# Kernel tuning notes

Measured on AMD Instinct MI355X. Metric: run time of the kernel, lower is better.

The kernel has to match this reference:

```python
import jax, jax.numpy as jnp
import numpy as np

R, C, N, E, H, F, ED, G, L = 1, 4, 50000, 200000, 128, 128, 16, 64, 2


def setup_inputs() -> dict:
    key = jax.random.key(0)
    ks = jax.random.split(key, 16)
    s = 0.05
    return {
        "x": jax.random.normal(ks[0], (R * C * N, H), jnp.float32),
        "batch": jnp.sort(jax.random.randint(ks[1], (N,), 0, G)),
        "edge_index": jax.random.randint(ks[2], (2, E), 0, N),
        "edge_attr": jax.random.normal(ks[3], (1, 1, E, ED), jnp.float32),
        "node_mask": jax.random.uniform(ks[4], (R, C, N, 1), jnp.float32),
        "edge_mask": jax.random.uniform(ks[5], (R, C, E, 1), jnp.float32),
        "W_be": jax.random.normal(ks[6], (ED, H), jnp.float32) * s,
        "b_be": jnp.zeros((H,), jnp.float32),
        "eps": jnp.zeros((L,), jnp.float32),
        "W1": jax.random.normal(ks[7], (L, H, H), jnp.float32) * s,
        "b1": jnp.zeros((L, H), jnp.float32),
        "W2": jax.random.normal(ks[8], (L, H, H), jnp.float32) * s,
        "b2": jnp.zeros((L, H), jnp.float32),
        "Wm1": jax.random.normal(ks[9], (H, H), jnp.float32) * s,
        "bm1": jnp.zeros((H,), jnp.float32),
        "Wm2": jax.random.normal(ks[10], (H, F), jnp.float32) * s,
        "bm2": jnp.zeros((F,), jnp.float32),
    }


def reference(x, batch, edge_index, edge_attr, node_mask, edge_mask,
              W_be, b_be, eps, W1, b1, W2, b2, Wm1, bm1, Wm2, bm2):
    gelu = lambda v: jax.nn.gelu(v, approximate=False)  # torch F.gelu default is erf
    src, dst = edge_index[0], edge_index[1]
    # bond encoder, shared across conv layers: (1,1,E,H)
    ee = edge_attr @ W_be + b_be
    for l in range(L):
        ux = x.reshape(R, C, N, H)
        # gather + add + GELU + edge-weight multiply: (R,C,E,H)
        msg = gelu(ux[:, :, src, :] + ee) * edge_mask
        # scatter_sum over edges into destination nodes
        agg = jnp.zeros_like(ux).at[:, :, dst, :].add(msg)
        h = (1.0 + eps[l]) * x + agg.reshape(x.shape)
        # conv MLP: Linear -> GELU -> Linear, then outer GELU (norm=Identity, dropout=0)
        h = gelu(h @ W1[l] + b1[l]) @ W2[l] + b2[l]
        x = gelu(h)
    # final node MLP (PyG MLP, norm=None): Linear -> GELU -> Linear
    x = gelu(x @ Wm1 + bm1) @ Wm2 + bm2  # (R*C*N, F)
    x4 = x.reshape(R, C, N, F)
    # masked mean-pool per (repeat, centroid, graph)
    num = jnp.zeros((R, C, G, F), x.dtype).at[:, :, batch, :].add(x4 * node_mask)
    den = jnp.zeros((R, C, G, 1), x.dtype).at[:, :, batch, :].add(node_mask) + 1e-7
    pooled = (num / den).transpose(0, 2, 1, 3).reshape(-1, F)  # (R*G*C, F)
    return pooled
```

## Files before the change

kernel.cpp:

```cpp
#include <hip/hip_runtime.h>
#include <math.h>

#define NN 50000
#define EN 200000
#define CC 4
#define HH 128
#define GG 64
#define LDSA 136
#define LDSF 132

typedef __attribute__((ext_vector_type(8))) short bs8;
typedef __attribute__((ext_vector_type(4))) float f32x4;
typedef __attribute__((ext_vector_type(2))) float f32x2;

__device__ __forceinline__ unsigned short f2bf(float f) {
  unsigned int u = __float_as_uint(f);
  u += 0x7FFFu + ((u >> 16) & 1u);
  return (unsigned short)(u >> 16);
}
__device__ __forceinline__ float bf2f(unsigned short h) {
  return __uint_as_float(((unsigned int)h) << 16);
}
__device__ __forceinline__ float gelu_f(float x) {
  float z = fabsf(x) * 0.7071067811865476f;
  float t = __builtin_amdgcn_rcpf(fmaf(0.3275911f, z, 1.0f));
  float poly = t * fmaf(t, fmaf(t, fmaf(t, fmaf(t, 1.061405429f, -1.453152027f),
                                        1.421413741f), -0.284496736f), 0.254829592f);
  float e = fmaf(-poly, __expf(-z * z), 1.0f);
  return 0.5f * x * (1.0f + copysignf(e, x));
}
__device__ __forceinline__ float gelu2_f(float x) {
  float z = fabsf(x) * 0.7071067811865476f;
  float t = __builtin_amdgcn_rcpf(fmaf(0.3275911f, z, 1.0f));
  float poly = t * fmaf(t, fmaf(t, fmaf(t, fmaf(t, 1.061405429f, -1.453152027f),
                                        1.421413741f), -0.284496736f), 0.254829592f);
  float e = fmaf(-poly, __expf(-z * z), 1.0f);
  return x * (1.0f + copysignf(e, x));
}

__global__ __launch_bounds__(256) void count_kernel(const int* __restrict__ dst,
                                                    int* __restrict__ counts) {
  int e = blockIdx.x * 256 + threadIdx.x;
  if (e < EN) atomicAdd(&counts[dst[e]], 1);
}

__global__ __launch_bounds__(256) void block_sum_kernel(const int* __restrict__ counts,
                                                        int* __restrict__ bsums) {
  int tid = threadIdx.x;
  int i = blockIdx.x * 256 + tid;
  int v = (i < NN) ? counts[i] : 0;
#pragma unroll
  for (int d = 1; d < 64; d <<= 1) v += __shfl_xor(v, d);
  __shared__ int ws4[4];
  if ((tid & 63) == 0) ws4[tid >> 6] = v;
  __syncthreads();
  if (tid == 0) bsums[blockIdx.x] = ws4[0] + ws4[1] + ws4[2] + ws4[3];
}

__global__ __launch_bounds__(256) void bsum_scan_kernel(const int* __restrict__ bsums,
                                                        int* __restrict__ boffs, int nb) {
  int tid = threadIdx.x, lane = tid & 63, wv = tid >> 6;
  int v = (tid < nb) ? bsums[tid] : 0;
  int s = v;
#pragma unroll
  for (int d = 1; d < 64; d <<= 1) { int t = __shfl_up(s, d); if (lane >= d) s += t; }
  __shared__ int wsum[4];
  if (lane == 63) wsum[wv] = s;
  __syncthreads();
  int pre = 0;
  for (int j = 0; j < wv; ++j) pre += wsum[j];
  if (tid < nb) boffs[tid] = pre + s - v;
}

__global__ __launch_bounds__(256) void block_scan_kernel(const int* __restrict__ counts,
                                                         const int* __restrict__ boffs,
                                                         int* __restrict__ offsets,
                                                         int* __restrict__ cursor) {
  int tid = threadIdx.x, lane = tid & 63, wv = tid >> 6;
  int i = blockIdx.x * 256 + tid;
  int v = (i < NN) ? counts[i] : 0;
  int s = v;
#pragma unroll
  for (int d = 1; d < 64; d <<= 1) { int t = __shfl_up(s, d); if (lane >= d) s += t; }
  __shared__ int wsum[4];
  if (lane == 63) wsum[wv] = s;
  __syncthreads();
  int pre = boffs[blockIdx.x];
  for (int j = 0; j < wv; ++j) pre += wsum[j];
  if (i < NN) { int e = pre + s - v; offsets[i] = e; cursor[i] = e; }
  if (i == 0) offsets[NN] = EN;
}

__global__ __launch_bounds__(256) void fill_kernel(const int* __restrict__ dst,
                                                   const int* __restrict__ src,
                                                   const float* __restrict__ emask,
                                                   int* __restrict__ cursor,
                                                   int2* __restrict__ csr_es,
                                                   float4* __restrict__ emask_s) {
  int e = blockIdx.x * 256 + threadIdx.x;
  if (e < EN) {
    int s = src[e];
    float m0 = emask[e];
    float m1 = emask[EN + e];
    float m2 = emask[2 * EN + e];
    float m3 = emask[3 * EN + e];
    int pos = atomicAdd(&cursor[dst[e]], 1);
    csr_es[pos] = make_int2(e, s);
    emask_s[pos] = make_float4(m0, m1, m2, m3);
  }
}

__global__ __launch_bounds__(256) void prep_w_kernel(const float* __restrict__ W1,
                                                     const float* __restrict__ W2,
                                                     const float* __restrict__ Wm1,
                                                     const float* __restrict__ Wm2,
                                                     unsigned short* __restrict__ wts) {
  int m = blockIdx.x >> 6;
  int idx = (blockIdx.x & 63) * 256 + threadIdx.x;
  const float* src = (m == 0) ? W1 : (m == 1) ? W1 + 16384 : (m == 2) ? W2
                     : (m == 3) ? W2 + 16384 : (m == 4) ? Wm1 : Wm2;
  unsigned short* dhi = wts + m * 32768;
  unsigned short* dlo = dhi + 16384;
  int n = idx >> 7, k = idx & 127;
  float v = src[k * HH + n];
  unsigned short hi = f2bf(v);
  dhi[n * HH + k] = hi;
  dlo[n * HH + k] = f2bf(v - bf2f(hi));
}

__global__ __launch_bounds__(256) void ee_kernel(const float* __restrict__ eattr,
                                                 const float* __restrict__ Wbe,
                                                 const float* __restrict__ bbe,
                                                 float* __restrict__ ee) {
  __shared__ float Ws[16 * HH];
  __shared__ float Ea[16 * 16];
  int tid = threadIdx.x;
  int e0 = blockIdx.x * 16;
#pragma unroll
  for (int i = 0; i < 8; ++i) Ws[tid + i * 256] = Wbe[tid + i * 256];
  Ea[tid] = eattr[(size_t)e0 * 16 + tid];
  __syncthreads();
  int h = tid & 127, half = tid >> 7;
  float bb = bbe[h];
#pragma unroll
  for (int j = 0; j < 8; ++j) {
    int el = j * 2 + half;
    float acc = bb;
#pragma unroll
    for (int d = 0; d < 16; ++d) acc += Ea[el * 16 + d] * Ws[d * HH + h];
    ee[(size_t)(e0 + el) * HH + h] = acc;
  }
}

__global__ __launch_bounds__(256) void agg_kernel(const float* __restrict__ x,
                                                  const float* __restrict__ ee,
                                                  const int* __restrict__ off,
                                                  const int2* __restrict__ csr_es,
                                                  const float4* __restrict__ emask_s,
                                                  const float* __restrict__ epsp, int layer,
                                                  float* __restrict__ hout) {
  int wv = threadIdx.x >> 6, lane = threadIdx.x & 63;
  int v = blockIdx.x * 4 + wv;
  int c2 = lane * 2;
  float2 acc[CC];
#pragma unroll
  for (int c = 0; c < CC; ++c) { acc[c].x = 0.f; acc[c].y = 0.f; }
  int beg = off[v], end = off[v + 1];

  float2 eeC; float2 xC[CC]; float emC[CC];
  int2 esN = make_int2(0, 0);
  eeC.x = 0.f; eeC.y = 0.f;
#pragma unroll
  for (int c = 0; c < CC; ++c) { xC[c].x = 0.f; xC[c].y = 0.f; emC[c] = 0.f; }

  if (beg < end) {
    int2 es0 = csr_es[beg];
    eeC = *(const float2*)(ee + (size_t)es0.x * HH + c2);
#pragma unroll
    for (int c = 0; c < CC; ++c)
      xC[c] = *(const float2*)(x + ((size_t)c * NN + es0.y) * HH + c2);
    float4 m = emask_s[beg];
    emC[0] = 0.5f * m.x; emC[1] = 0.5f * m.y; emC[2] = 0.5f * m.z; emC[3] = 0.5f * m.w;
    if (beg + 1 < end) esN = csr_es[beg + 1];
  }

  for (int t = beg; t < end; ++t) {
    float2 eeB; float2 xB[CC]; float emB[CC];
    int2 esNN = make_int2(0, 0);
    if (t + 1 < end) {
      eeB = *(const float2*)(ee + (size_t)esN.x * HH + c2);
#pragma unroll
      for (int c = 0; c < CC; ++c)
        xB[c] = *(const float2*)(x + ((size_t)c * NN + esN.y) * HH + c2);
      float4 m = emask_s[t + 1];
      emB[0] = 0.5f * m.x; emB[1] = 0.5f * m.y; emB[2] = 0.5f * m.z; emB[3] = 0.5f * m.w;
      if (t + 2 < end) esNN = csr_es[t + 2];
    } else {
      eeB.x = 0.f; eeB.y = 0.f;
#pragma unroll
      for (int c = 0; c < CC; ++c) { xB[c].x = 0.f; xB[c].y = 0.f; emB[c] = 0.f; }
    }
#pragma unroll
    for (int c = 0; c < CC; ++c) {
      acc[c].x += gelu2_f(xC[c].x + eeC.x) * emC[c];
      acc[c].y += gelu2_f(xC[c].y + eeC.y) * emC[c];
    }
    eeC = eeB;
#pragma unroll
    for (int c = 0; c < CC; ++c) { xC[c] = xB[c]; emC[c] = emB[c]; }
    esN = esNN;
  }

  float ep = 1.0f + epsp[layer];
#pragma unroll
  for (int c = 0; c < CC; ++c) {
    float2 xs = *(const float2*)(x + ((size_t)c * NN + v) * HH + c2);
    f32x2 o;
    o[0] = fmaf(ep, xs.x, acc[c].x);
    o[1] = fmaf(ep, xs.y, acc[c].y);
    __builtin_nontemporal_store(o, (f32x2*)(hout + ((size_t)c * NN + v) * HH + c2));
  }
}

__global__ __launch_bounds__(256, 2) void mlp_kernel(
    const float* __restrict__ in,
    const unsigned short* __restrict__ w1hi, const unsigned short* __restrict__ w1lo,
    const float* __restrict__ b1,
    const unsigned short* __restrict__ w2hi, const unsigned short* __restrict__ w2lo,
    const float* __restrict__ b2,
    float* __restrict__ out) {
  __shared__ __align__(16) unsigned short AB[2 * 64 * HH];
  unsigned short* Ahi = AB;
  unsigned short* Alo = AB + 64 * HH;
  int tid = threadIdx.x;
  int row0 = blockIdx.x * 64;
  int lane = tid & 63, wq = tid >> 6;
  int ln = lane & 15, quad = lane >> 4;

  bs8 b1h[4][2], b1l[4][2];
#pragma unroll
  for (int ks = 0; ks < 4; ++ks)
#pragma unroll
    for (int nt = 0; nt < 2; ++nt) {
      int wrow = ((wq * 2 + nt) * 16 + ln) * HH + ks * 32 + quad * 8;
      b1h[ks][nt] = *(const bs8*)(w1hi + wrow);
      b1l[ks][nt] = *(const bs8*)(w1lo + wrow);
    }

#pragma unroll
  for (int i = 0; i < 4; ++i) {
    int idx = tid + i * 256;
    int r = idx >> 4, blk = idx & 15;
    const float* p = in + (size_t)(row0 + r) * HH + blk * 8;
    f32x4 v0 = __builtin_nontemporal_load((const f32x4*)p);
    f32x4 v1 = __builtin_nontemporal_load((const f32x4*)(p + 4));
    bs8 h, l;
    h[0] = f2bf(v0[0]); h[1] = f2bf(v0[1]); h[2] = f2bf(v0[2]); h[3] = f2bf(v0[3]);
    h[4] = f2bf(v1[0]); h[5] = f2bf(v1[1]); h[6] = f2bf(v1[2]); h[7] = f2bf(v1[3]);
    l[0] = f2bf(v0[0] - bf2f(h[0])); l[1] = f2bf(v0[1] - bf2f(h[1]));
    l[2] = f2bf(v0[2] - bf2f(h[2])); l[3] = f2bf(v0[3] - bf2f(h[3]));
    l[4] = f2bf(v1[0] - bf2f(h[4])); l[5] = f2bf(v1[1] - bf2f(h[5]));
    l[6] = f2bf(v1[2] - bf2f(h[6])); l[7] = f2bf(v1[3] - bf2f(h[7]));
    int sb = blk ^ (r & 15);
    *(bs8*)(Ahi + r * HH + sb * 8) = h;
    *(bs8*)(Alo + r * HH + sb * 8) = l;
  }
  __syncthreads();

  f32x4 acc[4][2];
#pragma unroll
  for (int mt = 0; mt < 4; ++mt)
#pragma unroll
    for (int nt = 0; nt < 2; ++nt)
#pragma unroll
      for (int r = 0; r < 4; ++r) acc[mt][nt][r] = 0.f;
#pragma unroll
  for (int ks = 0; ks < 4; ++ks) {
    bs8 ah[4], al[4];
    int sb = ((ks * 4 + quad) ^ ln) * 8;
#pragma unroll
    for (int mt = 0; mt < 4; ++mt) {
      ah[mt] = *(const bs8*)(Ahi + (mt * 16 + ln) * HH + sb);
      al[mt] = *(const bs8*)(Alo + (mt * 16 + ln) * HH + sb);
    }
#pragma unroll
    for (int nt = 0; nt < 2; ++nt)
#pragma unroll
      for (int mt = 0; mt < 4; ++mt) {
        acc[mt][nt] = __builtin_amdgcn_mfma_f32_16x16x32_bf16(al[mt], b1h[ks][nt], acc[mt][nt], 0, 0, 0);
        acc[mt][nt] = __builtin_amdgcn_mfma_f32_16x16x32_bf16(ah[mt], b1l[ks][nt], acc[mt][nt], 0, 0, 0);
        acc[mt][nt] = __builtin_amdgcn_mfma_f32_16x16x32_bf16(ah[mt], b1h[ks][nt], acc[mt][nt], 0, 0, 0);
      }
  }
  __syncthreads();

  bs8 b2h[4][2], b2l[4][2];
#pragma unroll
  for (int ks = 0; ks < 4; ++ks)
#pragma unroll
    for (int nt = 0; nt < 2; ++nt) {
      int wrow = ((wq * 2 + nt) * 16 + ln) * HH + ks * 32 + quad * 8;
      b2h[ks][nt] = *(const bs8*)(w2hi + wrow);
      b2l[ks][nt] = *(const bs8*)(w2lo + wrow);
    }

#pragma unroll
  for (int nt = 0; nt < 2; ++nt) {
    int col = (wq * 2 + nt) * 16 + ln;
    int cb = col >> 3, co = col & 7;
    float bb = b1[col];
#pragma unroll
    for (int mt = 0; mt < 4; ++mt)
#pragma unroll
      for (int r = 0; r < 4; ++r) {
        float tv = gelu_f(acc[mt][nt][r] + bb);
        unsigned short th = f2bf(tv);
        int rr = mt * 16 + quad * 4 + r;
        int sof = rr * HH + (cb ^ (rr & 15)) * 8 + co;
        Ahi[sof] = th;
        Alo[sof] = f2bf(tv - bf2f(th));
      }
  }
  __syncthreads();

#pragma unroll
  for (int mt = 0; mt < 4; ++mt)
#pragma unroll
    for (int nt = 0; nt < 2; ++nt)
#pragma unroll
      for (int r = 0; r < 4; ++r) acc[mt][nt][r] = 0.f;
#pragma unroll
  for (int ks = 0; ks < 4; ++ks) {
    bs8 ah[4], al[4];
    int sb = ((ks * 4 + quad) ^ ln) * 8;
#pragma unroll
    for (int mt = 0; mt < 4; ++mt) {
      ah[mt] = *(const bs8*)(Ahi + (mt * 16 + ln) * HH + sb);
      al[mt] = *(const bs8*)(Alo + (mt * 16 + ln) * HH + sb);
    }
#pragma unroll
    for (int nt = 0; nt < 2; ++nt)
#pragma unroll
      for (int mt = 0; mt < 4; ++mt) {
        acc[mt][nt] = __builtin_amdgcn_mfma_f32_16x16x32_bf16(al[mt], b2h[ks][nt], acc[mt][nt], 0, 0, 0);
        acc[mt][nt] = __builtin_amdgcn_mfma_f32_16x16x32_bf16(ah[mt], b2l[ks][nt], acc[mt][nt], 0, 0, 0);
        acc[mt][nt] = __builtin_amdgcn_mfma_f32_16x16x32_bf16(ah[mt], b2h[ks][nt], acc[mt][nt], 0, 0, 0);
      }
  }
#pragma unroll
  for (int nt = 0; nt < 2; ++nt) {
    int col = (wq * 2 + nt) * 16 + ln;
    float bb = b2[col];
#pragma unroll
    for (int mt = 0; mt < 4; ++mt)
#pragma unroll
      for (int r = 0; r < 4; ++r) {
        float o = gelu_f(acc[mt][nt][r] + bb);
        out[(size_t)(row0 + mt * 16 + quad * 4 + r) * HH + col] = o;
      }
  }
}

__global__ __launch_bounds__(256, 2) void mlp_pool_kernel(
    const float* __restrict__ in,
    const unsigned short* __restrict__ w1hi, const unsigned short* __restrict__ w1lo,
    const float* __restrict__ b1,
    const unsigned short* __restrict__ w2hi, const unsigned short* __restrict__ w2lo,
    const float* __restrict__ b2,
    const float* __restrict__ nmask, const int* __restrict__ batch,
    float* __restrict__ num) {
  __shared__ __align__(16) unsigned short AB[128 * LDSA];
  __shared__ int kk[64];
  unsigned short* Ahi = AB;
  unsigned short* Alo = AB + 64 * LDSA;
  int tid = threadIdx.x;
  int row0 = blockIdx.x * 64;
  int lane = tid & 63, wq = tid >> 6;
  int ln = lane & 15, quad = lane >> 4;

  bs8 b1h[4][2], b1l[4][2];
#pragma unroll
  for (int ks = 0; ks < 4; ++ks)
#pragma unroll
    for (int nt = 0; nt < 2; ++nt) {
      int wrow = ((wq * 2 + nt) * 16 + ln) * HH + ks * 32 + quad * 8;
      b1h[ks][nt] = *(const bs8*)(w1hi + wrow);
      b1l[ks][nt] = *(const bs8*)(w1lo + wrow);
    }
#pragma unroll
  for (int i = 0; i < 8; ++i) {
    int idx = tid + i * 256;
    int r = idx >> 5, cc4 = idx & 31;
    f32x4 vv = __builtin_nontemporal_load(
        (const f32x4*)(in + (size_t)(row0 + r) * HH + cc4 * 4));
    unsigned short h0 = f2bf(vv[0]), h1 = f2bf(vv[1]), h2 = f2bf(vv[2]), h3 = f2bf(vv[3]);
    ushort4 hv; hv.x = h0; hv.y = h1; hv.z = h2; hv.w = h3;
    ushort4 lv;
    lv.x = f2bf(vv[0] - bf2f(h0)); lv.y = f2bf(vv[1] - bf2f(h1));
    lv.z = f2bf(vv[2] - bf2f(h2)); lv.w = f2bf(vv[3] - bf2f(h3));
    *(ushort4*)(Ahi + r * LDSA + cc4 * 4) = hv;
    *(ushort4*)(Alo + r * LDSA + cc4 * 4) = lv;
  }
  if (tid < 64) {
    int gr = row0 + tid;
    int c = gr / NN;
    int n = gr - c * NN;
    kk[tid] = (c << 6) | batch[n];
  }
  __syncthreads();

  f32x4 acc[4][2];
#pragma unroll
  for (int mt = 0; mt < 4; ++mt)
#pragma unroll
    for (int nt = 0; nt < 2; ++nt)
#pragma unroll
      for (int r = 0; r < 4; ++r) acc[mt][nt][r] = 0.f;
#pragma unroll
  for (int ks = 0; ks < 4; ++ks) {
    bs8 ah[4], al[4];
#pragma unroll
    for (int mt = 0; mt < 4; ++mt) {
      ah[mt] = *(const bs8*)(Ahi + (mt * 16 + ln) * LDSA + ks * 32 + quad * 8);
      al[mt] = *(const bs8*)(Alo + (mt * 16 + ln) * LDSA + ks * 32 + quad * 8);
    }
#pragma unroll
    for (int nt = 0; nt < 2; ++nt)
#pragma unroll
      for (int mt = 0; mt < 4; ++mt) {
        acc[mt][nt] = __builtin_amdgcn_mfma_f32_16x16x32_bf16(al[mt], b1h[ks][nt], acc[mt][nt], 0, 0, 0);
        acc[mt][nt] = __builtin_amdgcn_mfma_f32_16x16x32_bf16(ah[mt], b1l[ks][nt], acc[mt][nt], 0, 0, 0);
        acc[mt][nt] = __builtin_amdgcn_mfma_f32_16x16x32_bf16(ah[mt], b1h[ks][nt], acc[mt][nt], 0, 0, 0);
      }
  }
  __syncthreads();

  bs8 b2h[4][2], b2l[4][2];
#pragma unroll
  for (int ks = 0; ks < 4; ++ks)
#pragma unroll
    for (int nt = 0; nt < 2; ++nt) {
      int wrow = ((wq * 2 + nt) * 16 + ln) * HH + ks * 32 + quad * 8;
      b2h[ks][nt] = *(const bs8*)(w2hi + wrow);
      b2l[ks][nt] = *(const bs8*)(w2lo + wrow);
    }
#pragma unroll
  for (int nt = 0; nt < 2; ++nt) {
    int col = (wq * 2 + nt) * 16 + ln;
    float bb = b1[col];
#pragma unroll
    for (int mt = 0; mt < 4; ++mt)
#pragma unroll
      for (int r = 0; r < 4; ++r) {
        float tv = gelu_f(acc[mt][nt][r] + bb);
        unsigned short th = f2bf(tv);
        int rr = mt * 16 + quad * 4 + r;
        Ahi[rr * LDSA + col] = th;
        Alo[rr * LDSA + col] = f2bf(tv - bf2f(th));
      }
  }
  __syncthreads();

#pragma unroll
  for (int mt = 0; mt < 4; ++mt)
#pragma unroll
    for (int nt = 0; nt < 2; ++nt)
#pragma unroll
      for (int r = 0; r < 4; ++r) acc[mt][nt][r] = 0.f;
#pragma unroll
  for (int ks = 0; ks < 4; ++ks) {
    bs8 ah[4], al[4];
#pragma unroll
    for (int mt = 0; mt < 4; ++mt) {
      ah[mt] = *(const bs8*)(Ahi + (mt * 16 + ln) * LDSA + ks * 32 + quad * 8);
      al[mt] = *(const bs8*)(Alo + (mt * 16 + ln) * LDSA + ks * 32 + quad * 8);
    }
#pragma unroll
    for (int nt = 0; nt < 2; ++nt)
#pragma unroll
      for (int mt = 0; mt < 4; ++mt) {
        acc[mt][nt] = __builtin_amdgcn_mfma_f32_16x16x32_bf16(al[mt], b2h[ks][nt], acc[mt][nt], 0, 0, 0);
        acc[mt][nt] = __builtin_amdgcn_mfma_f32_16x16x32_bf16(ah[mt], b2l[ks][nt], acc[mt][nt], 0, 0, 0);
        acc[mt][nt] = __builtin_amdgcn_mfma_f32_16x16x32_bf16(ah[mt], b2h[ks][nt], acc[mt][nt], 0, 0, 0);
      }
  }
  __syncthreads();
  float* Tf = (float*)AB;
#pragma unroll
  for (int nt = 0; nt < 2; ++nt) {
    int col = (wq * 2 + nt) * 16 + ln;
    float bb = b2[col];
#pragma unroll
    for (int mt = 0; mt < 4; ++mt)
#pragma unroll
      for (int r = 0; r < 4; ++r) {
        int rl = mt * 16 + quad * 4 + r;
        int gr = row0 + rl;
        Tf[rl * LDSF + col] = (acc[mt][nt][r] + bb) * nmask[gr];
      }
  }
  __syncthreads();
  if (tid < 128) {
    int col = tid;
    float a2 = 0.f;
    int cur = kk[0];
    for (int r = 0; r < 64; ++r) {
      int k2 = kk[r];
      if (k2 != cur) {
        atomicAdd(&num[((size_t)(cur & 63) * CC + (cur >> 6)) * HH + col], a2);
        a2 = 0.f;
        cur = k2;
      }
      a2 += Tf[r * LDSF + col];
    }
    atomicAdd(&num[((size_t)(cur & 63) * CC + (cur >> 6)) * HH + col], a2);
  }
}

__global__ __launch_bounds__(256) void pool_finalize_kernel(const float* __restrict__ num,
                                                            const int* __restrict__ batch,
                                                            const float* __restrict__ nmask,
                                                            float* __restrict__ outp) {
  int g = blockIdx.x >> 2, c = blockIdx.x & 3;
  int lo = 0, hi = NN;
  while (lo < hi) { int m = (lo + hi) >> 1; if (batch[m] < g) lo = m + 1; else hi = m; }
  int start = lo;
  hi = NN;
  while (lo < hi) { int m = (lo + hi) >> 1; if (batch[m] < g + 1) lo = m + 1; else hi = m; }
  int end = lo;
  int tid = threadIdx.x;
  float d = 0.f;
  for (int n = start + tid; n < end; n += 256) d += nmask[c * NN + n];
#pragma unroll
  for (int k = 1; k < 64; k <<= 1) d += __shfl_xor(d, k);
  __shared__ float ws4[4];
  if ((tid & 63) == 0) ws4[tid >> 6] = d;
  __syncthreads();
  float den = ws4[0] + ws4[1] + ws4[2] + ws4[3] + 1e-7f;
  if (tid < 128) {
    int idx = blockIdx.x * 128 + tid;
    outp[idx] = num[idx] / den;
  }
}

extern "C" void kernel_launch(void* const* d_in, const int* in_sizes, int n_in,
                              void* d_out, int out_size, void* d_ws, size_t ws_size,
                              hipStream_t stream) {
  const float* x_in  = (const float*)d_in[0];
  const int*   batch = (const int*)d_in[1];
  const int*   eidx  = (const int*)d_in[2];
  const float* eattr = (const float*)d_in[3];
  const float* nmask = (const float*)d_in[4];
  const float* emask = (const float*)d_in[5];
  const float* Wbe   = (const float*)d_in[6];
  const float* bbe   = (const float*)d_in[7];
  const float* epsp  = (const float*)d_in[8];
  const float* W1    = (const float*)d_in[9];
  const float* b1    = (const float*)d_in[10];
  const float* W2    = (const float*)d_in[11];
  const float* b2    = (const float*)d_in[12];
  const float* Wm1   = (const float*)d_in[13];
  const float* bm1   = (const float*)d_in[14];
  const float* Wm2   = (const float*)d_in[15];
  const float* bm2   = (const float*)d_in[16];
  float* outp = (float*)d_out;

  const int* srcp = eidx;
  const int* dstp = eidx + EN;

  char* ws = (char*)d_ws;
  float* ee   = (float*)(ws);
  float* hbuf = (float*)(ws + 102400000);
  float* xbuf = (float*)(ws + 204800000);
  int* counts  = (int*)(ws + 307200000);
  int* offsets = (int*)(ws + 307400000);
  int* cursor  = (int*)(ws + 307600008);
  int2* csr_es = (int2*)(ws + 307800016);
  float4* emask_s = (float4*)(ws + 309400016);
  unsigned short* wts = (unsigned short*)(ws + 312600016);
  int* bsums = (int*)ws;
  int* boffs = (int*)(ws + 1024);
  float* num = (float*)ws;

  const int NB = (NN + 255) / 256;

  hipMemsetAsync(counts, 0, NN * sizeof(int), stream);
  count_kernel<<<(EN + 255) / 256, 256, 0, stream>>>(dstp, counts);
  block_sum_kernel<<<NB, 256, 0, stream>>>(counts, bsums);
  bsum_scan_kernel<<<1, 256, 0, stream>>>(bsums, boffs, NB);
  block_scan_kernel<<<NB, 256, 0, stream>>>(counts, boffs, offsets, cursor);
  fill_kernel<<<(EN + 255) / 256, 256, 0, stream>>>(dstp, srcp, emask, cursor, csr_es, emask_s);

  prep_w_kernel<<<384, 256, 0, stream>>>(W1, W2, Wm1, Wm2, wts);

  ee_kernel<<<EN / 16, 256, 0, stream>>>(eattr, Wbe, bbe, ee);

  agg_kernel<<<NN / 4, 256, 0, stream>>>(x_in, ee, offsets, csr_es, emask_s, epsp, 0, hbuf);
  mlp_kernel<<<(CC * NN) / 64, 256, 0, stream>>>(hbuf, wts + 0, wts + 16384, b1,
                                                 wts + 65536, wts + 81920, b2, xbuf);
  agg_kernel<<<NN / 4, 256, 0, stream>>>(xbuf, ee, offsets, csr_es, emask_s, epsp, 1, hbuf);
  mlp_kernel<<<(CC * NN) / 64, 256, 0, stream>>>(hbuf, wts + 32768, wts + 49152, b1 + 128,
                                                 wts + 98304, wts + 114688, b2 + 128, xbuf);
  hipMemsetAsync(num, 0, 131072, stream);
  mlp_pool_kernel<<<(CC * NN) / 64, 256, 0, stream>>>(xbuf, wts + 131072, wts + 147456, bm1,
                                                      wts + 163840, wts + 180224, bm2,
                                                      nmask, batch, num);
  pool_finalize_kernel<<<GG * CC, 256, 0, stream>>>(num, batch, nmask, outp);
}
```

Measured before the change: 717.2 us.

## Fuse edge aggregation and conv MLP into a single per-layer kernel

Merges the gather/GELU/scatter aggregation and the two-matmul conv MLP into one layer kernel. Each block aggregates 16 destination nodes across all 4 centroids, writes the result straight into shared memory as split bf16 hi/lo tiles, then runs both MFMA GEMMs. This drops the intermediate h buffer write and reread per layer and one launch per layer. The trade-off is that the irregular gather phase and the MFMA phase now share one block and its occupancy (launch bounds raised to 4), so latency hiding between them depends on co-resident blocks. The shared helpers loadW, zacc, gemm3 and tstage are factored out and reused in the pool kernel.

After: 678.5 us. -5.4%, faster.

```diff
diff --git a/kernel.cpp b/kernel.cpp
--- a/kernel.cpp
+++ b/kernel.cpp
@@ -152,78 +152,78 @@
   }
 }
 
-__global__ __launch_bounds__(256) void agg_kernel(const float* __restrict__ x,
-                                                  const float* __restrict__ ee,
-                                                  const int* __restrict__ off,
-                                                  const int2* __restrict__ csr_es,
-                                                  const float4* __restrict__ emask_s,
-                                                  const float* __restrict__ epsp, int layer,
-                                                  float* __restrict__ hout) {
-  int wv = threadIdx.x >> 6, lane = threadIdx.x & 63;
-  int v = blockIdx.x * 4 + wv;
-  int c2 = lane * 2;
-  float2 acc[CC];
-#pragma unroll
-  for (int c = 0; c < CC; ++c) { acc[c].x = 0.f; acc[c].y = 0.f; }
-  int beg = off[v], end = off[v + 1];
-
-  float2 eeC; float2 xC[CC]; float emC[CC];
-  int2 esN = make_int2(0, 0);
-  eeC.x = 0.f; eeC.y = 0.f;
-#pragma unroll
-  for (int c = 0; c < CC; ++c) { xC[c].x = 0.f; xC[c].y = 0.f; emC[c] = 0.f; }
-
-  if (beg < end) {
-    int2 es0 = csr_es[beg];
-    eeC = *(const float2*)(ee + (size_t)es0.x * HH + c2);
-#pragma unroll
-    for (int c = 0; c < CC; ++c)
-      xC[c] = *(const float2*)(x + ((size_t)c * NN + es0.y) * HH + c2);
-    float4 m = emask_s[beg];
-    emC[0] = 0.5f * m.x; emC[1] = 0.5f * m.y; emC[2] = 0.5f * m.z; emC[3] = 0.5f * m.w;
-    if (beg + 1 < end) esN = csr_es[beg + 1];
-  }
-
-  for (int t = beg; t < end; ++t) {
-    float2 eeB; float2 xB[CC]; float emB[CC];
-    int2 esNN = make_int2(0, 0);
-    if (t + 1 < end) {
-      eeB = *(const float2*)(ee + (size_t)esN.x * HH + c2);
-#pragma unroll
-      for (int c = 0; c < CC; ++c)
-        xB[c] = *(const float2*)(x + ((size_t)c * NN + esN.y) * HH + c2);
-      float4 m = emask_s[t + 1];
-      emB[0] = 0.5f * m.x; emB[1] = 0.5f * m.y; emB[2] = 0.5f * m.z; emB[3] = 0.5f * m.w;
-      if (t + 2 < end) esNN = csr_es[t + 2];
-    } else {
-      eeB.x = 0.f; eeB.y = 0.f;
-#pragma unroll
-      for (int c = 0; c < CC; ++c) { xB[c].x = 0.f; xB[c].y = 0.f; emB[c] = 0.f; }
-    }
-#pragma unroll
-    for (int c = 0; c < CC; ++c) {
-      acc[c].x += gelu2_f(xC[c].x + eeC.x) * emC[c];
-      acc[c].y += gelu2_f(xC[c].y + eeC.y) * emC[c];
-    }
-    eeC = eeB;
-#pragma unroll
-    for (int c = 0; c < CC; ++c) { xC[c] = xB[c]; emC[c] = emB[c]; }
-    esN = esNN;
-  }
-
-  float ep = 1.0f + epsp[layer];
-#pragma unroll
-  for (int c = 0; c < CC; ++c) {
-    float2 xs = *(const float2*)(x + ((size_t)c * NN + v) * HH + c2);
-    f32x2 o;
-    o[0] = fmaf(ep, xs.x, acc[c].x);
-    o[1] = fmaf(ep, xs.y, acc[c].y);
-    __builtin_nontemporal_store(o, (f32x2*)(hout + ((size_t)c * NN + v) * HH + c2));
-  }
-}
-
-__global__ __launch_bounds__(256, 2) void mlp_kernel(
-    const float* __restrict__ in,
+__device__ __forceinline__ void loadW(const unsigned short* __restrict__ whi,
+                                      const unsigned short* __restrict__ wlo,
+                                      bs8 (&bh)[4][2], bs8 (&bl)[4][2],
+                                      int ln, int quad, int wq) {
+#pragma unroll
+  for (int ks = 0; ks < 4; ++ks)
+#pragma unroll
+    for (int nt = 0; nt < 2; ++nt) {
+      int wrow = ((wq * 2 + nt) * 16 + ln) * HH + ks * 32 + quad * 8;
+      bh[ks][nt] = *(const bs8*)(whi + wrow);
+      bl[ks][nt] = *(const bs8*)(wlo + wrow);
+    }
+}
+__device__ __forceinline__ void zacc(f32x4 (&acc)[4][2]) {
+#pragma unroll
+  for (int mt = 0; mt < 4; ++mt)
+#pragma unroll
+    for (int nt = 0; nt < 2; ++nt)
+#pragma unroll
+      for (int r = 0; r < 4; ++r) acc[mt][nt][r] = 0.f;
+}
+__device__ __forceinline__ void gemm3(const unsigned short* Ahi, const unsigned short* Alo,
+                                      const bs8 (&bh)[4][2], const bs8 (&bl)[4][2],
+                                      f32x4 (&acc)[4][2], int ln, int quad) {
+#pragma unroll
+  for (int ks = 0; ks < 4; ++ks) {
+    bs8 ah[4], al[4];
+    int sb = ((ks * 4 + quad) ^ ln) * 8;
+#pragma unroll
+    for (int mt = 0; mt < 4; ++mt) {
+      ah[mt] = *(const bs8*)(Ahi + (mt * 16 + ln) * HH + sb);
+      al[mt] = *(const bs8*)(Alo + (mt * 16 + ln) * HH + sb);
+    }
+#pragma unroll
+    for (int nt = 0; nt < 2; ++nt)
+#pragma unroll
+      for (int mt = 0; mt < 4; ++mt) {
+        acc[mt][nt] = __builtin_amdgcn_mfma_f32_16x16x32_bf16(al[mt], bh[ks][nt], acc[mt][nt], 0, 0, 0);
+        acc[mt][nt] = __builtin_amdgcn_mfma_f32_16x16x32_bf16(ah[mt], bl[ks][nt], acc[mt][nt], 0, 0, 0);
+        acc[mt][nt] = __builtin_amdgcn_mfma_f32_16x16x32_bf16(ah[mt], bh[ks][nt], acc[mt][nt], 0, 0, 0);
+      }
+  }
+}
+__device__ __forceinline__ void tstage(unsigned short* Ahi, unsigned short* Alo,
+                                       const float* __restrict__ b1v, f32x4 (&acc)[4][2],
+                                       int ln, int quad, int wq) {
+#pragma unroll
+  for (int nt = 0; nt < 2; ++nt) {
+    int col = (wq * 2 + nt) * 16 + ln;
+    int cb = col >> 3, co = col & 7;
+    float bb = b1v[col];
+#pragma unroll
+    for (int mt = 0; mt < 4; ++mt)
+#pragma unroll
+      for (int r = 0; r < 4; ++r) {
+        float tv = gelu_f(acc[mt][nt][r] + bb);
+        unsigned short th = f2bf(tv);
+        int rr = mt * 16 + quad * 4 + r;
+        int sof = rr * HH + (cb ^ (rr & 15)) * 8 + co;
+        Ahi[sof] = th;
+        Alo[sof] = f2bf(tv - bf2f(th));
+      }
+  }
+}
+
+__global__ __launch_bounds__(256, 4) void layer_kernel(
+    const float* __restrict__ x,
+    const float* __restrict__ ee,
+    const int* __restrict__ off,
+    const int2* __restrict__ csr_es,
+    const float4* __restrict__ emask_s,
+    const float* __restrict__ epsp, int layer,
     const unsigned short* __restrict__ w1hi, const unsigned short* __restrict__ w1lo,
     const float* __restrict__ b1,
     const unsigned short* __restrict__ w2hi, const unsigned short* __restrict__ w2lo,
@@ -233,120 +233,98 @@
   unsigned short* Ahi = AB;
   unsigned short* Alo = AB + 64 * HH;
   int tid = threadIdx.x;
-  int row0 = blockIdx.x * 64;
   int lane = tid & 63, wq = tid >> 6;
   int ln = lane & 15, quad = lane >> 4;
-
-  bs8 b1h[4][2], b1l[4][2];
-#pragma unroll
-  for (int ks = 0; ks < 4; ++ks)
-#pragma unroll
-    for (int nt = 0; nt < 2; ++nt) {
-      int wrow = ((wq * 2 + nt) * 16 + ln) * HH + ks * 32 + quad * 8;
-      b1h[ks][nt] = *(const bs8*)(w1hi + wrow);
-      b1l[ks][nt] = *(const bs8*)(w1lo + wrow);
-    }
-
-#pragma unroll
-  for (int i = 0; i < 4; ++i) {
-    int idx = tid + i * 256;
-    int r = idx >> 4, blk = idx & 15;
-    const float* p = in + (size_t)(row0 + r) * HH + blk * 8;
-    f32x4 v0 = __builtin_nontemporal_load((const f32x4*)p);
-    f32x4 v1 = __builtin_nontemporal_load((const f32x4*)(p + 4));
-    bs8 h, l;
-    h[0] = f2bf(v0[0]); h[1] = f2bf(v0[1]); h[2] = f2bf(v0[2]); h[3] = f2bf(v0[3]);
-    h[4] = f2bf(v1[0]); h[5] = f2bf(v1[1]); h[6] = f2bf(v1[2]); h[7] = f2bf(v1[3]);
-    l[0] = f2bf(v0[0] - bf2f(h[0])); l[1] = f2bf(v0[1] - bf2f(h[1]));
-    l[2] = f2bf(v0[2] - bf2f(h[2])); l[3] = f2bf(v0[3] - bf2f(h[3]));
-    l[4] = f2bf(v1[0] - bf2f(h[4])); l[5] = f2bf(v1[1] - bf2f(h[5]));
-    l[6] = f2bf(v1[2] - bf2f(h[6])); l[7] = f2bf(v1[3] - bf2f(h[7]));
-    int sb = blk ^ (r & 15);
-    *(bs8*)(Ahi + r * HH + sb * 8) = h;
-    *(bs8*)(Alo + r * HH + sb * 8) = l;
-  }
+  int n0 = blockIdx.x * 16;
+  int c2 = lane * 2;
+  float ep = 1.0f + epsp[layer];
+  int blk = lane >> 2;
+  int wo = (lane & 3) * 2;
+
+  for (int j = 0; j < 4; ++j) {
+    int nn = wq * 4 + j;
+    int v = n0 + nn;
+    float2 acc[CC];
+#pragma unroll
+    for (int c = 0; c < CC; ++c) { acc[c].x = 0.f; acc[c].y = 0.f; }
+    int beg = off[v], end = off[v + 1];
+
+    float2 eeC; float2 xC[CC]; float emC[CC];
+    int2 esN = make_int2(0, 0);
+    eeC.x = 0.f; eeC.y = 0.f;
+#pragma unroll
+    for (int c = 0; c < CC; ++c) { xC[c].x = 0.f; xC[c].y = 0.f; emC[c] = 0.f; }
+
+    if (beg < end) {
+      int2 es0 = csr_es[beg];
+      eeC = *(const float2*)(ee + (size_t)es0.x * HH + c2);
+#pragma unroll
+      for (int c = 0; c < CC; ++c)
+        xC[c] = *(const float2*)(x + ((size_t)c * NN + es0.y) * HH + c2);
+      float4 m = emask_s[beg];
+      emC[0] = 0.5f * m.x; emC[1] = 0.5f * m.y; emC[2] = 0.5f * m.z; emC[3] = 0.5f * m.w;
+      if (beg + 1 < end) esN = csr_es[beg + 1];
+    }
+
+    for (int t = beg; t < end; ++t) {
+      float2 eeB; float2 xB[CC]; float emB[CC];
+      int2 esNN = make_int2(0, 0);
+      if (t + 1 < end) {
+        eeB = *(const float2*)(ee + (size_t)esN.x * HH + c2);
+#pragma unroll
+        for (int c = 0; c < CC; ++c)
+          xB[c] = *(const float2*)(x + ((size_t)c * NN + esN.y) * HH + c2);
+        float4 m = emask_s[t + 1];
+        emB[0] = 0.5f * m.x; emB[1] = 0.5f * m.y; emB[2] = 0.5f * m.z; emB[3] = 0.5f * m.w;
+        if (t + 2 < end) esNN = csr_es[t + 2];
+      } else {
+        eeB.x = 0.f; eeB.y = 0.f;
+#pragma unroll
+        for (int c = 0; c < CC; ++c) { xB[c].x = 0.f; xB[c].y = 0.f; emB[c] = 0.f; }
+      }
+#pragma unroll
+      for (int c = 0; c < CC; ++c) {
+        acc[c].x += gelu2_f(xC[c].x + eeC.x) * emC[c];
+        acc[c].y += gelu2_f(xC[c].y + eeC.y) * emC[c];
+      }
+      eeC = eeB;
+#pragma unroll
+      for (int c = 0; c < CC; ++c) { xC[c] = xB[c]; emC[c] = emB[c]; }
+      esN = esNN;
+    }
+
+#pragma unroll
+    for (int c = 0; c < CC; ++c) {
+      float2 xs = *(const float2*)(x + ((size_t)c * NN + v) * HH + c2);
+      float o0 = fmaf(ep, xs.x, acc[c].x);
+      float o1 = fmaf(ep, xs.y, acc[c].y);
+      int rr = c * 16 + nn;
+      int base = rr * HH + ((blk ^ (rr & 15)) * 8) + wo;
+      unsigned short h0 = f2bf(o0), h1 = f2bf(o1);
+      ushort2 hv; hv.x = h0; hv.y = h1;
+      ushort2 lv; lv.x = f2bf(o0 - bf2f(h0)); lv.y = f2bf(o1 - bf2f(h1));
+      *(ushort2*)(Ahi + base) = hv;
+      *(ushort2*)(Alo + base) = lv;
+    }
+  }
+
+  bs8 w1h[4][2], w1l[4][2];
+  loadW(w1hi, w1lo, w1h, w1l, ln, quad, wq);
   __syncthreads();
 
   f32x4 acc[4][2];
-#pragma unroll
-  for (int mt = 0; mt < 4; ++mt)
-#pragma unroll
-    for (int nt = 0; nt < 2; ++nt)
-#pragma unroll
-      for (int r = 0; r < 4; ++r) acc[mt][nt][r] = 0.f;
-#pragma unroll
-  for (int ks = 0; ks < 4; ++ks) {
-    bs8 ah[4], al[4];
-    int sb = ((ks * 4 + quad) ^ ln) * 8;
-#pragma unroll
-    for (int mt = 0; mt < 4; ++mt) {
-      ah[mt] = *(const bs8*)(Ahi + (mt * 16 + ln) * HH + sb);
-      al[mt] = *(const bs8*)(Alo + (mt * 16 + ln) * HH + sb);
-    }
-#pragma unroll
-    for (int nt = 0; nt < 2; ++nt)
-#pragma unroll
-      for (int mt = 0; mt < 4; ++mt) {
-        acc[mt][nt] = __builtin_amdgcn_mfma_f32_16x16x32_bf16(al[mt], b1h[ks][nt], acc[mt][nt], 0, 0, 0);
-        acc[mt][nt] = __builtin_amdgcn_mfma_f32_16x16x32_bf16(ah[mt], b1l[ks][nt], acc[mt][nt], 0, 0, 0);
-        acc[mt][nt] = __builtin_amdgcn_mfma_f32_16x16x32_bf16(ah[mt], b1h[ks][nt], acc[mt][nt], 0, 0, 0);
-      }
-  }
-  __syncthreads();
-
-  bs8 b2h[4][2], b2l[4][2];
-#pragma unroll
-  for (int ks = 0; ks < 4; ++ks)
-#pragma unroll
-    for (int nt = 0; nt < 2; ++nt) {
-      int wrow = ((wq * 2 + nt) * 16 + ln) * HH + ks * 32 + quad * 8;
-      b2h[ks][nt] = *(const bs8*)(w2hi + wrow);
-      b2l[ks][nt] = *(const bs8*)(w2lo + wrow);
-    }
-
-#pragma unroll
-  for (int nt = 0; nt < 2; ++nt) {
-    int col = (wq * 2 + nt) * 16 + ln;
-    int cb = col >> 3, co = col & 7;
-    float bb = b1[col];
-#pragma unroll
-    for (int mt = 0; mt < 4; ++mt)
-#pragma unroll
-      for (int r = 0; r < 4; ++r) {
-        float tv = gelu_f(acc[mt][nt][r] + bb);
-        unsigned short th = f2bf(tv);
-        int rr = mt * 16 + quad * 4 + r;
-        int sof = rr * HH + (cb ^ (rr & 15)) * 8 + co;
-        Ahi[sof] = th;
-        Alo[sof] = f2bf(tv - bf2f(th));
-      }
-  }
-  __syncthreads();
-
-#pragma unroll
-  for (int mt = 0; mt < 4; ++mt)
-#pragma unroll
-    for (int nt = 0; nt < 2; ++nt)
-#pragma unroll
-      for (int r = 0; r < 4; ++r) acc[mt][nt][r] = 0.f;
-#pragma unroll
-  for (int ks = 0; ks < 4; ++ks) {
-    bs8 ah[4], al[4];
-    int sb = ((ks * 4 + quad) ^ ln) * 8;
-#pragma unroll
-    for (int mt = 0; mt < 4; ++mt) {
-      ah[mt] = *(const bs8*)(Ahi + (mt * 16 + ln) * HH + sb);
-      al[mt] = *(const bs8*)(Alo + (mt * 16 + ln) * HH + sb);
-    }
-#pragma unroll
-    for (int nt = 0; nt < 2; ++nt)
-#pragma unroll
-      for (int mt = 0; mt < 4; ++mt) {
-        acc[mt][nt] = __builtin_amdgcn_mfma_f32_16x16x32_bf16(al[mt], b2h[ks][nt], acc[mt][nt], 0, 0, 0);
-        acc[mt][nt] = __builtin_amdgcn_mfma_f32_16x16x32_bf16(ah[mt], b2l[ks][nt], acc[mt][nt], 0, 0, 0);
-        acc[mt][nt] = __builtin_amdgcn_mfma_f32_16x16x32_bf16(ah[mt], b2h[ks][nt], acc[mt][nt], 0, 0, 0);
-      }
-  }
+  zacc(acc);
+  gemm3(Ahi, Alo, w1h, w1l, acc, ln, quad);
+  __syncthreads();
+
+  bs8 w2h[4][2], w2l[4][2];
+  loadW(w2hi, w2lo, w2h, w2l, ln, quad, wq);
+  tstage(Ahi, Alo, b1, acc, ln, quad, wq);
+  __syncthreads();
+
+  zacc(acc);
+  gemm3(Ahi, Alo, w2h, w2l, acc, ln, quad);
+
 #pragma unroll
   for (int nt = 0; nt < 2; ++nt) {
     int col = (wq * 2 + nt) * 16 + ln;
@@ -356,7 +334,7 @@
 #pragma unroll
       for (int r = 0; r < 4; ++r) {
         float o = gelu_f(acc[mt][nt][r] + bb);
-        out[(size_t)(row0 + mt * 16 + quad * 4 + r) * HH + col] = o;
+        out[((size_t)mt * NN + n0 + quad * 4 + r) * HH + col] = o;
       }
   }
 }
@@ -379,14 +357,7 @@
   int ln = lane & 15, quad = lane >> 4;
 
   bs8 b1h[4][2], b1l[4][2];
-#pragma unroll
-  for (int ks = 0; ks < 4; ++ks)
-#pragma unroll
-    for (int nt = 0; nt < 2; ++nt) {
-      int wrow = ((wq * 2 + nt) * 16 + ln) * HH + ks * 32 + quad * 8;
-      b1h[ks][nt] = *(const bs8*)(w1hi + wrow);
-      b1l[ks][nt] = *(const bs8*)(w1lo + wrow);
-    }
+  loadW(w1hi, w1lo, b1h, b1l, ln, quad, wq);
 #pragma unroll
   for (int i = 0; i < 8; ++i) {
     int idx = tid + i * 256;
@@ -410,12 +381,7 @@
   __syncthreads();
 
   f32x4 acc[4][2];
-#pragma unroll
-  for (int mt = 0; mt < 4; ++mt)
-#pragma unroll
-    for (int nt = 0; nt < 2; ++nt)
-#pragma unroll
-      for (int r = 0; r < 4; ++r) acc[mt][nt][r] = 0.f;
+  zacc(acc);
 #pragma unroll
   for (int ks = 0; ks < 4; ++ks) {
     bs8 ah[4], al[4];
@@ -436,14 +402,7 @@
   __syncthreads();
 
   bs8 b2h[4][2], b2l[4][2];
-#pragma unroll
-  for (int ks = 0; ks < 4; ++ks)
-#pragma unroll
-    for (int nt = 0; nt < 2; ++nt) {
-      int wrow = ((wq * 2 + nt) * 16 + ln) * HH + ks * 32 + quad * 8;
-      b2h[ks][nt] = *(const bs8*)(w2hi + wrow);
-      b2l[ks][nt] = *(const bs8*)(w2lo + wrow);
-    }
+  loadW(w2hi, w2lo, b2h, b2l, ln, quad, wq);
 #pragma unroll
   for (int nt = 0; nt < 2; ++nt) {
     int col = (wq * 2 + nt) * 16 + ln;
@@ -461,12 +420,7 @@
   }
   __syncthreads();
 
-#pragma unroll
-  for (int mt = 0; mt < 4; ++mt)
-#pragma unroll
-    for (int nt = 0; nt < 2; ++nt)
-#pragma unroll
-      for (int r = 0; r < 4; ++r) acc[mt][nt][r] = 0.f;
+  zacc(acc);
 #pragma unroll
   for (int ks = 0; ks < 4; ++ks) {
     bs8 ah[4], al[4];
@@ -595,12 +549,12 @@
 
   ee_kernel<<<EN / 16, 256, 0, stream>>>(eattr, Wbe, bbe, ee);
 
-  agg_kernel<<<NN / 4, 256, 0, stream>>>(x_in, ee, offsets, csr_es, emask_s, epsp, 0, hbuf);
-  mlp_kernel<<<(CC * NN) / 64, 256, 0, stream>>>(hbuf, wts + 0, wts + 16384, b1,
-                                                 wts + 65536, wts + 81920, b2, xbuf);
-  agg_kernel<<<NN / 4, 256, 0, stream>>>(xbuf, ee, offsets, csr_es, emask_s, epsp, 1, hbuf);
-  mlp_kernel<<<(CC * NN) / 64, 256, 0, stream>>>(hbuf, wts + 32768, wts + 49152, b1 + 128,
-                                                 wts + 98304, wts + 114688, b2 + 128, xbuf);
+  layer_kernel<<<NN / 16, 256, 0, stream>>>(x_in, ee, offsets, csr_es, emask_s, epsp, 0,
+                                            wts + 0, wts + 16384, b1,
+                                            wts + 65536, wts + 81920, b2, hbuf);
+  layer_kernel<<<NN / 16, 256, 0, stream>>>(hbuf, ee, offsets, csr_es, emask_s, epsp, 1,
+                                            wts + 32768, wts + 49152, b1 + 128,
+                                            wts + 98304, wts + 114688, b2 + 128, xbuf);
   hipMemsetAsync(num, 0, 131072, stream);
   mlp_pool_kernel<<<(CC * NN) / 64, 256, 0, stream>>>(xbuf, wts + 131072, wts + 147456, bm1,
                                                       wts + 163840, wts + 180224, bm2,
```
